# Optimization experiments

Hardware: AMD Instinct MI355X
Metric: run time of the kernel (lower is better)

The kernel has to match this reference:

```python
import jax, jax.numpy as jnp
import numpy as np

N_HEADS = 16
HIDDEN = 1024
HEAD = HIDDEN // N_HEADS


def setup_inputs() -> dict:
    key = jax.random.key(0)
    ks = jax.random.split(key, 11)
    B, S, H = 2, 2048, HIDDEN
    s = 1.0 / np.sqrt(H)
    return {
        "query": jax.random.normal(ks[0], (B, S, H), jnp.float32),
        "key": jax.random.normal(ks[1], (B, S, H), jnp.float32),
        "value": jax.random.normal(ks[2], (B, S, H), jnp.float32),
        "Wq": jax.random.normal(ks[3], (H, H), jnp.float32) * s,
        "bq": jnp.zeros((H,), jnp.float32),
        "Wk": jax.random.normal(ks[4], (H, H), jnp.float32) * s,
        "bk": jnp.zeros((H,), jnp.float32),
        "Wv": jax.random.normal(ks[5], (H, H), jnp.float32) * s,
        "bv": jnp.zeros((H,), jnp.float32),
        "Wo": jax.random.normal(ks[6], (H, H), jnp.float32) * s,
        "bo": jnp.zeros((H,), jnp.float32),
    }


def reference(query, key, value, Wq, bq, Wk, bk, Wv, bv, Wo, bo):
    B, Sq, H = query.shape
    Sk = key.shape[1]
    # QKV projections, split heads: [B, n_heads, S, head]
    q = (query @ Wq + bq).reshape(B, Sq, N_HEADS, HEAD).transpose(0, 2, 1, 3)
    k = (key @ Wk + bk).reshape(B, Sk, N_HEADS, HEAD).transpose(0, 2, 1, 3)
    v = (value @ Wv + bv).reshape(B, Sk, N_HEADS, HEAD).transpose(0, 2, 1, 3)
    # scaled dot-product attention (no mask, dropout p=0)
    scores = jnp.einsum("bhqd,bhkd->bhqk", q, k) / np.sqrt(HEAD).astype(np.float32)
    attn = jax.nn.softmax(scores, axis=-1)
    out = jnp.einsum("bhqk,bhkd->bhqd", attn, v)
    out = out.transpose(0, 2, 1, 3).reshape(B, Sq, H)
    return out @ Wo + bo
```

## Files before the change

kernel.cpp:

```cpp
#include <hip/hip_runtime.h>
#include <hip/hip_bf16.h>
#include <stdint.h>

typedef unsigned short u16;
typedef short bf16x8 __attribute__((ext_vector_type(8)));
typedef float f32x4 __attribute__((ext_vector_type(4)));

#define DEVI static __device__ __forceinline__

#if __has_builtin(__builtin_amdgcn_exp2f)
#define EXP2F(x) __builtin_amdgcn_exp2f(x)
#else
#define EXP2F(x) exp2f(x)
#endif

DEVI u16 f2bf(float f) {
  union { float f; uint32_t u; } v; v.f = f;
  uint32_t u = v.u;
  u += 0x7fffu + ((u >> 16) & 1u);
  return (u16)(u >> 16);
}
DEVI uint32_t pk2bf(float lo, float hi) {
  __hip_bfloat162 h = __float22bfloat162_rn(float2{lo, hi});
  union { __hip_bfloat162 h; uint32_t u; } v; v.h = h; return v.u;
}

DEVI void async16(const void* g, const void* l) {
  __builtin_amdgcn_global_load_lds(
      (const __attribute__((address_space(1))) void*)g,
      (__attribute__((address_space(3))) void*)l, 16, 0, 0);
}

DEVI f32x4 mfma16(bf16x8 a, bf16x8 b, f32x4 c) {
  return __builtin_amdgcn_mfma_f32_16x16x32_bf16(a, b, c, 0, 0, 0);
}

#define CSC 0.18033688011112042f

__global__ void prep(const float* __restrict__ q, const float* __restrict__ k,
                     const float* __restrict__ v,
                     const float* __restrict__ Wq, const float* __restrict__ Wk,
                     const float* __restrict__ Wv, const float* __restrict__ Wo,
                     u16* __restrict__ XB, u16* __restrict__ WT) {
  __shared__ u16 tile[64 * 68];
  const int bid = blockIdx.x, t = threadIdx.x;
  if (bid < 12288) {
    const int z = bid >> 12, x = bid & 4095;
    const float* src = (z == 0) ? q : (z == 1) ? k : v;
    const int i = (x * 256 + t) * 4;
    float4 f = *(const float4*)(src + i);
    ushort4 o;
    o.x = f2bf(f.x); o.y = f2bf(f.y); o.z = f2bf(f.z); o.w = f2bf(f.w);
    *(ushort4*)(XB + (size_t)z * 4194304 + i) = o;
  } else {
    const int j = bid - 12288;
    const int z = j >> 8, rem = j & 255;
    const float* W = (z == 0) ? Wq : (z == 1) ? Wk : (z == 2) ? Wv : Wo;
    u16* out = WT + (size_t)z * 1048576;
    const int R0 = (rem >> 4) * 64, C0 = (rem & 15) * 64;
#pragma unroll
    for (int it = 0; it < 16; ++it) {
      int jj = it * 256 + t;
      int r = jj >> 6, c = jj & 63;
      tile[r * 68 + c] = f2bf(W[(size_t)(R0 + r) * 1024 + C0 + c]);
    }
    __syncthreads();
#pragma unroll
    for (int it = 0; it < 16; ++it) {
      int jj = it * 256 + t;
      int c = jj >> 6, r = jj & 63;
      out[(size_t)(C0 + c) * 1024 + R0 + r] = tile[r * 68 + c];
    }
  }
}

__global__ __launch_bounds__(256, 3)
void qkv_gemm(const u16* __restrict__ XB, const u16* __restrict__ WT,
              const float* __restrict__ bq, const float* __restrict__ bk,
              const float* __restrict__ bv,
              u16* __restrict__ QN, u16* __restrict__ KN, u16* __restrict__ VT) {
  __shared__ u16 smem[16896];
  u16* lA = smem;
  u16* lB = smem + 8192;
  const int z = blockIdx.y;
  const u16* A  = XB + (size_t)z * 4194304;
  const u16* Bt = WT + (size_t)z * 1048576;
  const float* bias = (z == 0) ? bq : (z == 1) ? bk : bv;
  const int T = blockIdx.x;
  const int m0 = (T & 31) * 128, n0 = (T >> 5) * 128;
  const int t = threadIdx.x, lane = t & 63, w = t >> 6;
  const int quad = lane >> 4, l16 = lane & 15;
  const int wm = (w & 1) * 64, wn = (w >> 1) * 64;

  f32x4 acc[4][4] = {};
  for (int kt = 0; kt < 16; ++kt) {
    const int k0 = kt * 64;
#pragma unroll
    for (int it = 0; it < 4; ++it) {
      int i = it * 256 + t;
      int r = i >> 3, cc = i & 7, c = cc ^ (r & 7);
      async16(A + (size_t)(m0 + r) * 1024 + k0 + c * 8, &lA[i * 8]);
      async16(Bt + (size_t)(n0 + r) * 1024 + k0 + c * 8, &lB[i * 8]);
    }
    __syncthreads();
#pragma unroll
    for (int ks = 0; ks < 2; ++ks) {
      bf16x8 af[4], bfr[4];
#pragma unroll
      for (int rt = 0; rt < 4; ++rt) {
        int row = wm + rt * 16 + l16;
        af[rt] = *(const bf16x8*)&lA[row * 64 + ((ks * 4 + quad) ^ (row & 7)) * 8];
      }
#pragma unroll
      for (int ct = 0; ct < 4; ++ct) {
        int row = wn + ct * 16 + l16;
        bfr[ct] = *(const bf16x8*)&lB[row * 64 + ((ks * 4 + quad) ^ (row & 7)) * 8];
      }
#pragma unroll
      for (int rt = 0; rt < 4; ++rt)
#pragma unroll
        for (int ct = 0; ct < 4; ++ct)
          acc[rt][ct] = mfma16(bfr[ct], af[rt], acc[rt][ct]);
    }
    __syncthreads();
  }

  if (z < 2) {
    const float scl = (z == 0) ? CSC : 1.0f;
#pragma unroll
    for (int rt = 0; rt < 4; ++rt) {
      int sl = wm + rt * 16 + l16;
#pragma unroll
      for (int ct = 0; ct < 4; ++ct) {
        int nb = wn + ct * 16 + quad * 4;
        float4 b4 = *(const float4*)&bias[n0 + nb];
        ushort4 pk;
        pk.x = f2bf((acc[rt][ct][0] + b4.x) * scl);
        pk.y = f2bf((acc[rt][ct][1] + b4.y) * scl);
        pk.z = f2bf((acc[rt][ct][2] + b4.z) * scl);
        pk.w = f2bf((acc[rt][ct][3] + b4.w) * scl);
        *(ushort4*)&smem[sl * 132 + nb] = pk;
      }
    }
    __syncthreads();
    u16* out = (z == 0) ? QN : KN;
#pragma unroll
    for (int p = 0; p < 8; ++p) {
      int idx = p * 256 + t;
      int row = idx >> 4, chunk = idx & 15;
      *(bf16x8*)&out[(size_t)(m0 + row) * 1024 + n0 + chunk * 8] =
          *(const bf16x8*)&smem[row * 132 + chunk * 8];
    }
  } else {
#pragma unroll
    for (int rt = 0; rt < 4; ++rt) {
      int sl = wm + rt * 16 + l16;
#pragma unroll
      for (int ct = 0; ct < 4; ++ct) {
        int nb = wn + ct * 16 + quad * 4;
        float4 b4 = *(const float4*)&bias[n0 + nb];
        smem[(nb + 0) * 132 + sl] = f2bf(acc[rt][ct][0] + b4.x);
        smem[(nb + 1) * 132 + sl] = f2bf(acc[rt][ct][1] + b4.y);
        smem[(nb + 2) * 132 + sl] = f2bf(acc[rt][ct][2] + b4.z);
        smem[(nb + 3) * 132 + sl] = f2bf(acc[rt][ct][3] + b4.w);
      }
    }
    __syncthreads();
    const int bb = m0 >> 11, sb = m0 & 2047;
#pragma unroll
    for (int p = 0; p < 8; ++p) {
      int idx = p * 256 + t;
      int dl = idx >> 4, chunk = idx & 15;
      int ncol = n0 + dl, hh = ncol >> 6, dd = ncol & 63;
      *(bf16x8*)&VT[((size_t)((bb * 16 + hh) * 64 + dd)) * 2048 + sb + chunk * 8] =
          *(const bf16x8*)&smem[dl * 132 + chunk * 8];
    }
  }
}

__global__ __launch_bounds__(512, 4)
void attn11(const u16* __restrict__ QN, const u16* __restrict__ KN,
            const u16* __restrict__ VT, u16* __restrict__ AO) {
  __shared__ u16 lK[4][64 * 64];
  __shared__ u16 lV[4][64 * 64];
  const int qt0 = blockIdx.x, h = blockIdx.y, b = blockIdx.z;
  const int t = threadIdx.x, lane = t & 63, w = t >> 6;
  const int quad = lane >> 4, l16 = lane & 15;
  const u16* Qg = QN + ((size_t)(b * 2048 + qt0 * 128)) * 1024 + h * 64;
  const u16* Kg = KN + ((size_t)b * 2048) * 1024 + h * 64;
  const u16* Vg = VT + ((size_t)((b * 16 + h) * 64)) * 2048;

  const int sr_r = t >> 3;
  const int sg_r = (sr_r & 0x23) | ((sr_r & 8) << 1) | ((sr_r & 4) << 1) |
                   ((sr_r & 16) >> 2);
  const int sc_c = (t & 7) ^ (sr_r & 7);

  bf16x8 qf[2];
#pragma unroll
  for (int ks = 0; ks < 2; ++ks)
    qf[ks] = *(const bf16x8*)(Qg + (size_t)(w * 16 + l16) * 1024 + ks * 32 + quad * 8);

  const bf16x8 ones = {0x3F80, 0x3F80, 0x3F80, 0x3F80,
                       0x3F80, 0x3F80, 0x3F80, 0x3F80};

  async16(Kg + (size_t)sg_r * 1024 + sc_c * 8, &lK[0][t * 8]);
  async16(Vg + (size_t)sr_r * 2048 + sc_c * 8, &lV[0][t * 8]);
  async16(Kg + (size_t)(64 + sg_r) * 1024 + sc_c * 8, &lK[1][t * 8]);
  async16(Vg + (size_t)sr_r * 2048 + 64 + sc_c * 8, &lV[1][t * 8]);

  f32x4 o[4] = {};
  f32x4 ls = {};

  for (int it = 0; it < 16; ++it) {
    const int ta = it * 2;
    asm volatile("s_waitcnt vmcnt(0)" ::: "memory");
    __builtin_amdgcn_s_barrier();
    __builtin_amdgcn_sched_barrier(0);

    if (it + 1 < 16) {
      const int kb0 = (ta + 2) * 64, nb0 = (ta + 2) & 3;
      async16(Kg + (size_t)(kb0 + sg_r) * 1024 + sc_c * 8, &lK[nb0][t * 8]);
      async16(Vg + (size_t)sr_r * 2048 + kb0 + sc_c * 8, &lV[nb0][t * 8]);
      const int kb1 = (ta + 3) * 64, nb1 = (ta + 3) & 3;
      async16(Kg + (size_t)(kb1 + sg_r) * 1024 + sc_c * 8, &lK[nb1][t * 8]);
      async16(Vg + (size_t)sr_r * 2048 + kb1 + sc_c * 8, &lV[nb1][t * 8]);
    }

    f32x4 sc2[2][4];
    __builtin_amdgcn_s_setprio(1);
#pragma unroll
    for (int u = 0; u < 2; ++u) {
      const u16* Kc = &lK[(ta + u) & 3][0];
#pragma unroll
      for (int st = 0; st < 4; ++st) {
        int row = st * 16 + l16;
        bf16x8 kf0 = *(const bf16x8*)&Kc[row * 64 + ((quad) ^ (row & 7)) * 8];
        bf16x8 kf1 = *(const bf16x8*)&Kc[row * 64 + ((4 + quad) ^ (row & 7)) * 8];
        f32x4 z = {};
        sc2[u][st] = mfma16(kf0, qf[0], z);
        sc2[u][st] = mfma16(kf1, qf[1], sc2[u][st]);
      }
    }
    __builtin_amdgcn_s_setprio(0);

#pragma unroll
    for (int u = 0; u < 2; ++u) {
      union { uint32_t uw[4]; bf16x8 v; } p0, p1;
#pragma unroll
      for (int st = 0; st < 2; ++st) {
        p0.uw[st * 2 + 0] = pk2bf(EXP2F(sc2[u][st][0]), EXP2F(sc2[u][st][1]));
        p0.uw[st * 2 + 1] = pk2bf(EXP2F(sc2[u][st][2]), EXP2F(sc2[u][st][3]));
        p1.uw[st * 2 + 0] = pk2bf(EXP2F(sc2[u][2 + st][0]), EXP2F(sc2[u][2 + st][1]));
        p1.uw[st * 2 + 1] = pk2bf(EXP2F(sc2[u][2 + st][2]), EXP2F(sc2[u][2 + st][3]));
      }
      __builtin_amdgcn_s_setprio(1);
      ls = mfma16(ones, p0.v, ls);
      ls = mfma16(ones, p1.v, ls);
      const u16* Vc = &lV[(ta + u) & 3][0];
#pragma unroll
      for (int dt = 0; dt < 4; ++dt) {
        int row = dt * 16 + l16;
        bf16x8 vf0 = *(const bf16x8*)&Vc[row * 64 + ((quad) ^ (row & 7)) * 8];
        bf16x8 vf1 = *(const bf16x8*)&Vc[row * 64 + ((4 + quad) ^ (row & 7)) * 8];
        o[dt] = mfma16(vf0, p0.v, o[dt]);
        o[dt] = mfma16(vf1, p1.v, o[dt]);
      }
      __builtin_amdgcn_s_setprio(0);
    }
  }

  float inv = 1.0f / ls[0];
  int qglob = qt0 * 128 + w * 16 + l16;
  size_t base = ((size_t)(b * 2048 + qglob)) * 1024 + h * 64;
#pragma unroll
  for (int dt = 0; dt < 4; ++dt) {
    ushort4 pk;
    pk.x = f2bf(o[dt][0] * inv);
    pk.y = f2bf(o[dt][1] * inv);
    pk.z = f2bf(o[dt][2] * inv);
    pk.w = f2bf(o[dt][3] * inv);
    *(ushort4*)&AO[base + dt * 16 + quad * 4] = pk;
  }
}

__global__ __launch_bounds__(256, 4)
void oproj_gemm(const u16* __restrict__ AO, const u16* __restrict__ Bt,
                const float* __restrict__ bias, float* __restrict__ out) {
  __shared__ u16 lA[128 * 64];
  __shared__ u16 lB[64 * 64];
  const int T = blockIdx.x;
  const int m0 = (T & 31) * 128, n0 = (T >> 5) * 64;
  const int t = threadIdx.x, lane = t & 63, w = t >> 6;
  const int quad = lane >> 4, l16 = lane & 15;
  const int wm = (w & 1) * 64, wn = (w >> 1) * 32;

  f32x4 acc[4][2] = {};
  for (int kt = 0; kt < 16; ++kt) {
    const int k0 = kt * 64;
#pragma unroll
    for (int it = 0; it < 4; ++it) {
      int i = it * 256 + t;
      int r = i >> 3, cc = i & 7, c = cc ^ (r & 7);
      async16(AO + (size_t)(m0 + r) * 1024 + k0 + c * 8, &lA[i * 8]);
    }
#pragma unroll
    for (int it = 0; it < 2; ++it) {
      int i = it * 256 + t;
      int r = i >> 3, cc = i & 7, c = cc ^ (r & 7);
      async16(Bt + (size_t)(n0 + r) * 1024 + k0 + c * 8, &lB[i * 8]);
    }
    __syncthreads();
#pragma unroll
    for (int ks = 0; ks < 2; ++ks) {
      bf16x8 af[4], bfr[2];
#pragma unroll
      for (int rt = 0; rt < 4; ++rt) {
        int row = wm + rt * 16 + l16;
        af[rt] = *(const bf16x8*)&lA[row * 64 + ((ks * 4 + quad) ^ (row & 7)) * 8];
      }
#pragma unroll
      for (int ct = 0; ct < 2; ++ct) {
        int row = wn + ct * 16 + l16;
        bfr[ct] = *(const bf16x8*)&lB[row * 64 + ((ks * 4 + quad) ^ (row & 7)) * 8];
      }
#pragma unroll
      for (int rt = 0; rt < 4; ++rt)
#pragma unroll
        for (int ct = 0; ct < 2; ++ct)
          acc[rt][ct] = mfma16(af[rt], bfr[ct], acc[rt][ct]);
    }
    __syncthreads();
  }

#pragma unroll
  for (int ct = 0; ct < 2; ++ct) {
    int ncol = n0 + wn + ct * 16 + l16;
    float bvv = bias[ncol];
#pragma unroll
    for (int rt = 0; rt < 4; ++rt)
#pragma unroll
      for (int r = 0; r < 4; ++r) {
        int m = m0 + wm + rt * 16 + quad * 4 + r;
        out[(size_t)m * 1024 + ncol] = acc[rt][ct][r] + bvv;
      }
  }
}

extern "C" void kernel_launch(void* const* d_in, const int* in_sizes, int n_in,
                              void* d_out, int out_size, void* d_ws, size_t ws_size,
                              hipStream_t stream) {
  const float* query = (const float*)d_in[0];
  const float* key   = (const float*)d_in[1];
  const float* value = (const float*)d_in[2];
  const float* Wq = (const float*)d_in[3];
  const float* bq = (const float*)d_in[4];
  const float* Wk = (const float*)d_in[5];
  const float* bk = (const float*)d_in[6];
  const float* Wv = (const float*)d_in[7];
  const float* bv = (const float*)d_in[8];
  const float* Wo = (const float*)d_in[9];
  const float* bo = (const float*)d_in[10];
  float* out = (float*)d_out;

  u16* WT = (u16*)d_ws;
  u16* QN = WT + 4 * 1048576;
  u16* KN = QN + 4194304;
  u16* VT = KN + 4194304;
  u16* XB = VT + 4194304;
  u16* AO = XB;

  prep<<<dim3(13312), 256, 0, stream>>>(query, key, value, Wq, Wk, Wv, Wo, XB, WT);
  qkv_gemm<<<dim3(256, 3), 256, 0, stream>>>(XB, WT, bq, bk, bv, QN, KN, VT);
  attn11<<<dim3(16, 16, 2), 512, 0, stream>>>(QN, KN, VT, AO);
  oproj_gemm<<<dim3(512), 256, 0, stream>>>(AO, WT + 3 * 1048576, bo, out);
}
```

Measured before the change: 217.7 us.

## Double-buffer LDS tiles in QKV and output projection GEMMs

Both projection GEMMs now keep two shared-memory buffers. The next K tile is issued with async loads before the MFMAs on the current tile run, so global-memory latency overlaps with compute. The change also raises wave priority around the MFMA blocks and lowers launch-bounds occupancy to make room for the doubled LDS. The risk is fewer resident blocks per CU, which may hurt latency hiding. The attention kernel, which likely dominates the runtime, is untouched.

```diff
diff --git a/kernel.cpp b/kernel.cpp
--- a/kernel.cpp
+++ b/kernel.cpp
@@ -74,14 +74,23 @@
   }
 }
 
-__global__ __launch_bounds__(256, 3)
+DEVI void qstage(const u16* __restrict__ A, const u16* __restrict__ Bt,
+                 u16* lA, u16* lB, int m0, int n0, int k0, int t) {
+#pragma unroll
+  for (int it = 0; it < 4; ++it) {
+    int i = it * 256 + t;
+    int r = i >> 3, cc = i & 7, c = cc ^ (r & 7);
+    async16(A + (size_t)(m0 + r) * 1024 + k0 + c * 8, &lA[i * 8]);
+    async16(Bt + (size_t)(n0 + r) * 1024 + k0 + c * 8, &lB[i * 8]);
+  }
+}
+
+__global__ __launch_bounds__(256, 2)
 void qkv_gemm(const u16* __restrict__ XB, const u16* __restrict__ WT,
               const float* __restrict__ bq, const float* __restrict__ bk,
               const float* __restrict__ bv,
               u16* __restrict__ QN, u16* __restrict__ KN, u16* __restrict__ VT) {
-  __shared__ u16 smem[16896];
-  u16* lA = smem;
-  u16* lB = smem + 8192;
+  __shared__ u16 smem[32768];
   const int z = blockIdx.y;
   const u16* A  = XB + (size_t)z * 4194304;
   const u16* Bt = WT + (size_t)z * 1048576;
@@ -92,17 +101,19 @@
   const int quad = lane >> 4, l16 = lane & 15;
   const int wm = (w & 1) * 64, wn = (w >> 1) * 64;
 
+  qstage(A, Bt, smem, smem + 8192, m0, n0, 0, t);
+
   f32x4 acc[4][4] = {};
   for (int kt = 0; kt < 16; ++kt) {
-    const int k0 = kt * 64;
-#pragma unroll
-    for (int it = 0; it < 4; ++it) {
-      int i = it * 256 + t;
-      int r = i >> 3, cc = i & 7, c = cc ^ (r & 7);
-      async16(A + (size_t)(m0 + r) * 1024 + k0 + c * 8, &lA[i * 8]);
-      async16(Bt + (size_t)(n0 + r) * 1024 + k0 + c * 8, &lB[i * 8]);
-    }
-    __syncthreads();
+    asm volatile("s_waitcnt vmcnt(0)" ::: "memory");
+    __builtin_amdgcn_s_barrier();
+    __builtin_amdgcn_sched_barrier(0);
+    if (kt + 1 < 16) {
+      u16* nb = smem + ((kt + 1) & 1) * 16384;
+      qstage(A, Bt, nb, nb + 8192, m0, n0, (kt + 1) * 64, t);
+    }
+    const u16* lA = smem + (kt & 1) * 16384;
+    const u16* lB = lA + 8192;
 #pragma unroll
     for (int ks = 0; ks < 2; ++ks) {
       bf16x8 af[4], bfr[4];
@@ -116,14 +127,16 @@
         int row = wn + ct * 16 + l16;
         bfr[ct] = *(const bf16x8*)&lB[row * 64 + ((ks * 4 + quad) ^ (row & 7)) * 8];
       }
+      __builtin_amdgcn_s_setprio(1);
 #pragma unroll
       for (int rt = 0; rt < 4; ++rt)
 #pragma unroll
         for (int ct = 0; ct < 4; ++ct)
           acc[rt][ct] = mfma16(bfr[ct], af[rt], acc[rt][ct]);
-    }
-    __syncthreads();
-  }
+      __builtin_amdgcn_s_setprio(0);
+    }
+  }
+  __syncthreads();
 
   if (z < 2) {
     const float scl = (z == 0) ? CSC : 1.0f;
@@ -283,33 +296,56 @@
   }
 }
 
-__global__ __launch_bounds__(256, 4)
+__global__ __launch_bounds__(256, 3)
 void oproj_gemm(const u16* __restrict__ AO, const u16* __restrict__ Bt,
                 const float* __restrict__ bias, float* __restrict__ out) {
-  __shared__ u16 lA[128 * 64];
-  __shared__ u16 lB[64 * 64];
+  __shared__ u16 smem[24576];
   const int T = blockIdx.x;
   const int m0 = (T & 31) * 128, n0 = (T >> 5) * 64;
   const int t = threadIdx.x, lane = t & 63, w = t >> 6;
   const int quad = lane >> 4, l16 = lane & 15;
   const int wm = (w & 1) * 64, wn = (w >> 1) * 32;
 
-  f32x4 acc[4][2] = {};
-  for (int kt = 0; kt < 16; ++kt) {
-    const int k0 = kt * 64;
+  {
+    u16* lA = smem; u16* lB = smem + 8192;
 #pragma unroll
     for (int it = 0; it < 4; ++it) {
       int i = it * 256 + t;
       int r = i >> 3, cc = i & 7, c = cc ^ (r & 7);
-      async16(AO + (size_t)(m0 + r) * 1024 + k0 + c * 8, &lA[i * 8]);
+      async16(AO + (size_t)(m0 + r) * 1024 + c * 8, &lA[i * 8]);
     }
 #pragma unroll
     for (int it = 0; it < 2; ++it) {
       int i = it * 256 + t;
       int r = i >> 3, cc = i & 7, c = cc ^ (r & 7);
-      async16(Bt + (size_t)(n0 + r) * 1024 + k0 + c * 8, &lB[i * 8]);
-    }
-    __syncthreads();
+      async16(Bt + (size_t)(n0 + r) * 1024 + c * 8, &lB[i * 8]);
+    }
+  }
+
+  f32x4 acc[4][2] = {};
+  for (int kt = 0; kt < 16; ++kt) {
+    asm volatile("s_waitcnt vmcnt(0)" ::: "memory");
+    __builtin_amdgcn_s_barrier();
+    __builtin_amdgcn_sched_barrier(0);
+    if (kt + 1 < 16) {
+      const int k0 = (kt + 1) * 64;
+      u16* lA = smem + ((kt + 1) & 1) * 12288;
+      u16* lB = lA + 8192;
+#pragma unroll
+      for (int it = 0; it < 4; ++it) {
+        int i = it * 256 + t;
+        int r = i >> 3, cc = i & 7, c = cc ^ (r & 7);
+        async16(AO + (size_t)(m0 + r) * 1024 + k0 + c * 8, &lA[i * 8]);
+      }
+#pragma unroll
+      for (int it = 0; it < 2; ++it) {
+        int i = it * 256 + t;
+        int r = i >> 3, cc = i & 7, c = cc ^ (r & 7);
+        async16(Bt + (size_t)(n0 + r) * 1024 + k0 + c * 8, &lB[i * 8]);
+      }
+    }
+    const u16* lA = smem + (kt & 1) * 12288;
+    const u16* lB = lA + 8192;
 #pragma unroll
     for (int ks = 0; ks < 2; ++ks) {
       bf16x8 af[4], bfr[2];
@@ -323,13 +359,14 @@
         int row = wn + ct * 16 + l16;
         bfr[ct] = *(const bf16x8*)&lB[row * 64 + ((ks * 4 + quad) ^ (row & 7)) * 8];
       }
+      __builtin_amdgcn_s_setprio(1);
 #pragma unroll
       for (int rt = 0; rt < 4; ++rt)
 #pragma unroll
         for (int ct = 0; ct < 2; ++ct)
           acc[rt][ct] = mfma16(af[rt], bfr[ct], acc[rt][ct]);
-    }
-    __syncthreads();
+      __builtin_amdgcn_s_setprio(0);
+    }
   }
 
 #pragma unroll
```

Measured after the change: 203.0 us, median of 2. 1.07x faster.
